# Kernel optimization log

Hardware: AMD Instinct MI355X
Metric: run time of the kernel (lower is better)

The kernel has to match this reference:

```python
import jax, jax.numpy as jnp
import numpy as np

B, L, NIN, NHID, NLAYERS = 16, 2048, 1024, 1024, 2


def _gru_step_zero_h(x, W_ih, b_ih, W_hh, b_hh):
    """torch GRU cell with h_prev = 0 (faithful to the module's bug where
    hidden is never updated and starts at zeros).
    r = sigmoid(W_ir x + b_ir + b_hr)
    z = sigmoid(W_iz x + b_iz + b_hz)
    n = tanh(W_in x + b_in + r * b_hn)   # W_hn @ 0 == 0
    h = (1 - z) * n                       # + z * 0
    W_hh is unused because h_prev == 0 (kept as an arg for parity).
    """
    del W_hh
    g = jnp.einsum('blf,hf->blh', x, W_ih) + b_ih  # (B, L, 3H)
    H = b_ih.shape[0] // 3
    gi_r, gi_z, gi_n = g[..., :H], g[..., H:2 * H], g[..., 2 * H:]
    bh_r, bh_z, bh_n = b_hh[:H], b_hh[H:2 * H], b_hh[2 * H:]
    r = jax.nn.sigmoid(gi_r + bh_r)
    z = jax.nn.sigmoid(gi_z + bh_z)
    n = jnp.tanh(gi_n + r * bh_n)
    return (1.0 - z) * n


def setup_inputs() -> dict:
    key = jax.random.key(0)
    ks = jax.random.split(key, 12)
    s_in = 1.0 / np.sqrt(NIN)
    s_h = 1.0 / np.sqrt(NHID)
    inp = {
        'inputs': jax.random.normal(ks[0], (B, L, NIN), dtype=jnp.float32),
        'inputs_mask': jax.random.randint(ks[1], (B, L), 0, 2, dtype=jnp.int32),
        # layer 0 (input size NIN)
        'W_ih0': jax.random.uniform(ks[2], (3 * NHID, NIN), jnp.float32, -s_in, s_in),
        'W_hh0': jax.random.uniform(ks[3], (3 * NHID, NHID), jnp.float32, -s_h, s_h),
        'b_ih0': jax.random.uniform(ks[4], (3 * NHID,), jnp.float32, -s_h, s_h),
        'b_hh0': jax.random.uniform(ks[5], (3 * NHID,), jnp.float32, -s_h, s_h),
        # layer 1 (input size NHID)
        'W_ih1': jax.random.uniform(ks[6], (3 * NHID, NHID), jnp.float32, -s_h, s_h),
        'W_hh1': jax.random.uniform(ks[7], (3 * NHID, NHID), jnp.float32, -s_h, s_h),
        'b_ih1': jax.random.uniform(ks[8], (3 * NHID,), jnp.float32, -s_h, s_h),
        'b_hh1': jax.random.uniform(ks[9], (3 * NHID,), jnp.float32, -s_h, s_h),
    }
    return inp


def reference(inputs, inputs_mask, W_ih0, W_hh0, b_ih0, b_hh0,
              W_ih1, W_hh1, b_ih1, b_hh1):
    # hidden is never updated in the original step(), so every timestep runs
    # the 2-layer GRU one step from zero hidden -> fully parallel over time.
    h1 = _gru_step_zero_h(inputs, W_ih0, b_ih0, W_hh0, b_hh0)   # (B, L, H)
    h2 = _gru_step_zero_h(h1, W_ih1, b_ih1, W_hh1, b_hh1)       # (B, L, H)
    mask = inputs_mask.astype(h2.dtype)[..., None]               # (B, L, 1)
    # output_p * mask + hidden[0] * (1 - mask), with hidden[0] == 0
    out = h2 * mask
    # original returns (steps, b_s, nhid)
    return jnp.transpose(out, (1, 0, 2))
```

## Files before the change

### kernel.cpp

```cpp
#include <hip/hip_runtime.h>
#include <hip/hip_bf16.h>
#include <cstdint>
#include <cstddef>

#define BB 16
#define LL 2048
#define MM (BB * LL)
#define KK 1024
#define HH 1024

typedef __attribute__((ext_vector_type(8))) short bf16x8;
typedef __attribute__((ext_vector_type(4))) float f32x4;

__device__ __forceinline__ unsigned short f2bf(float f) {
    unsigned u = __builtin_bit_cast(unsigned, f);
    u += 0x7fffu + ((u >> 16) & 1u);
    return (unsigned short)(u >> 16);
}

__global__ void cvt_f32_to_bf16(const float* __restrict__ in,
                                unsigned short* __restrict__ out, int n8) {
    int i = blockIdx.x * blockDim.x + threadIdx.x;
    if (i >= n8) return;
    const float4* p = reinterpret_cast<const float4*>(in) + (size_t)i * 2;
    float4 v0 = p[0];
    float4 v1 = p[1];
    union { unsigned short us[8]; uint4 v; } o;
    o.us[0] = f2bf(v0.x); o.us[1] = f2bf(v0.y);
    o.us[2] = f2bf(v0.z); o.us[3] = f2bf(v0.w);
    o.us[4] = f2bf(v1.x); o.us[5] = f2bf(v1.y);
    o.us[6] = f2bf(v1.z); o.us[7] = f2bf(v1.w);
    reinterpret_cast<uint4*>(out)[i] = o.v;
}

__global__ __launch_bounds__(1024) void scan_mask(const int* __restrict__ mask,
                                                  int* __restrict__ rows,
                                                  int* __restrict__ Na) {
    __shared__ int psum[1024];
    const int t = threadIdx.x;
    const int base = t * 32;
    int m[32];
    int cnt = 0;
#pragma unroll
    for (int i = 0; i < 32; ++i) { m[i] = mask[base + i]; cnt += (m[i] != 0); }
    psum[t] = cnt;
    __syncthreads();
    for (int off = 1; off < 1024; off <<= 1) {
        int v = (t >= off) ? psum[t - off] : 0;
        __syncthreads();
        psum[t] += v;
        __syncthreads();
    }
    int offset = psum[t] - cnt;
#pragma unroll
    for (int i = 0; i < 32; ++i) {
        if (m[i]) rows[offset++] = base + i;
    }
    if (t == 1023) *Na = psum[1023];
}

__global__ __launch_bounds__(256) void gather_cvt(const float* __restrict__ x,
                                                  const int* __restrict__ rows,
                                                  const int* __restrict__ Na,
                                                  unsigned short* __restrict__ xbf) {
    const int j = blockIdx.x;
    if (j >= *Na) return;
    const int r = rows[j];
    const float4 v = reinterpret_cast<const float4*>(x + (size_t)r * KK)[threadIdx.x];
    ushort4 o;
    o.x = f2bf(v.x); o.y = f2bf(v.y); o.z = f2bf(v.z); o.w = f2bf(v.w);
    reinterpret_cast<ushort4*>(xbf + (size_t)j * KK)[threadIdx.x] = o;
}

__global__ __launch_bounds__(256) void zero_masked(const int* __restrict__ mask,
                                                   float* __restrict__ out) {
    const int m = blockIdx.x;
    if (mask[m] != 0) return;
    const int bb = m >> 11;
    const int ll = m & 2047;
    float4 z = {0.f, 0.f, 0.f, 0.f};
    reinterpret_cast<float4*>(out + ((size_t)ll * BB + bb) * HH)[threadIdx.x] = z;
}

__device__ __forceinline__ void gload16(const unsigned short* g, unsigned short* l) {
    __builtin_amdgcn_global_load_lds(
        (const __attribute__((address_space(1))) unsigned int*)g,
        (__attribute__((address_space(3))) unsigned int*)l,
        16, 0, 0);
}

#define WAITVM0  asm volatile("s_waitcnt vmcnt(0)" ::: "memory")
#define SB       __builtin_amdgcn_sched_barrier(0)
#define BAR      __builtin_amdgcn_s_barrier()

template <int MODE>
__global__ __launch_bounds__(256, 3) void gru_layer(
    const unsigned short* __restrict__ A,
    const unsigned short* __restrict__ W,
    const float* __restrict__ b_ih,
    const float* __restrict__ b_hh,
    const int* __restrict__ rows,
    const int* __restrict__ Na_p,
    unsigned short* __restrict__ out_bf,
    float* __restrict__ out_f) {
    __shared__ unsigned short lds[2][10240];

    const int Na = *Na_p;
    const int m0 = blockIdx.x * 128;
    if (m0 >= Na) return;
    const int n0 = blockIdx.y * 64;

    const int tid  = threadIdx.x;
    const int lane = tid & 63;
    const int wid  = tid >> 6;
    const int wr   = wid >> 1;
    const int wc   = wid & 1;

    const int trow = tid >> 2;
    const int tcol = ((tid & 3) ^ ((trow >> 1) & 3)) * 8;
    int r0 = m0 + trow;        if (r0 >= Na) r0 = Na - 1;
    int r1 = m0 + 64 + trow;   if (r1 >= Na) r1 = Na - 1;
    const unsigned short* a0 = A + (size_t)r0 * KK + tcol;
    const unsigned short* a1 = A + (size_t)r1 * KK + tcol;
    const unsigned short* b0 = W + (size_t)(0 * HH + n0 + trow) * KK + tcol;
    const unsigned short* b1 = W + (size_t)(1 * HH + n0 + trow) * KK + tcol;
    const unsigned short* b2 = W + (size_t)(2 * HH + n0 + trow) * KK + tcol;

#define STAGE(kt, c) do {                                        \
        const int _o = (kt) * 32;                                \
        unsigned short* _L = &lds[(c)][wid * 512];               \
        gload16(a0 + _o, _L + 0 * 2048);                         \
        gload16(a1 + _o, _L + 1 * 2048);                         \
        gload16(b0 + _o, _L + 2 * 2048);                         \
        gload16(b1 + _o, _L + 3 * 2048);                         \
        gload16(b2 + _o, _L + 4 * 2048);                         \
    } while (0)

    const int l15 = lane & 15;
    const int akp = (((lane >> 4) ^ (lane >> 1)) & 3) << 3;
    int aoff[4], boff[2];
#pragma unroll
    for (int mf = 0; mf < 4; ++mf)
        aoff[mf] = (wr * 64 + mf * 16 + l15) * 32 + akp;
#pragma unroll
    for (int nf = 0; nf < 2; ++nf)
        boff[nf] = 4096 + (wc * 32 + nf * 16 + l15) * 32 + akp;

    f32x4 accr[4][2] = {};
    f32x4 accz[4][2] = {};
    f32x4 accn[4][2] = {};

#define COMPUTE(Lp) do {                                                          \
        bf16x8 af[4];                                                             \
        _Pragma("unroll") for (int mf = 0; mf < 4; ++mf)                          \
            af[mf] = *reinterpret_cast<const bf16x8*>(&(Lp)[aoff[mf]]);           \
        _Pragma("unroll") for (int nf = 0; nf < 2; ++nf) {                        \
            bf16x8 br  = *reinterpret_cast<const bf16x8*>(&(Lp)[boff[nf]]);       \
            bf16x8 bz  = *reinterpret_cast<const bf16x8*>(&(Lp)[boff[nf] + 2048]);\
            bf16x8 bnn = *reinterpret_cast<const bf16x8*>(&(Lp)[boff[nf] + 4096]);\
            __builtin_amdgcn_s_setprio(1);                                        \
            _Pragma("unroll") for (int mf = 0; mf < 4; ++mf) {                    \
                accr[mf][nf] = __builtin_amdgcn_mfma_f32_16x16x32_bf16(           \
                    af[mf], br,  accr[mf][nf], 0, 0, 0);                          \
                accz[mf][nf] = __builtin_amdgcn_mfma_f32_16x16x32_bf16(           \
                    af[mf], bz,  accz[mf][nf], 0, 0, 0);                          \
                accn[mf][nf] = __builtin_amdgcn_mfma_f32_16x16x32_bf16(           \
                    af[mf], bnn, accn[mf][nf], 0, 0, 0);                          \
            }                                                                     \
            __builtin_amdgcn_s_setprio(0);                                        \
        }                                                                         \
    } while (0)

    STAGE(0, 0);
    WAITVM0; BAR; SB;

    int cur = 0;
#pragma unroll 1
    for (int kt = 0; kt < 31; ++kt) {
        STAGE(kt + 1, cur ^ 1);
        const unsigned short* L = &lds[cur][0];
        COMPUTE(L);
        WAITVM0; BAR; SB;
        cur ^= 1;
    }
    {
        const unsigned short* L = &lds[cur][0];
        COMPUTE(L);
    }

#pragma unroll
    for (int nf = 0; nf < 2; ++nf) {
        const int col = n0 + wc * 32 + nf * 16 + l15;
        const float br_b = b_ih[col] + b_hh[col];
        const float bz_b = b_ih[HH + col] + b_hh[HH + col];
        const float bn_i = b_ih[2 * HH + col];
        const float bn_h = b_hh[2 * HH + col];
#pragma unroll
        for (int mf = 0; mf < 4; ++mf) {
#pragma unroll
            for (int j = 0; j < 4; ++j) {
                const int row = m0 + wr * 64 + mf * 16 + (lane >> 4) * 4 + j;
                if (row >= Na) continue;
                const float r = 1.f / (1.f + __expf(-(accr[mf][nf][j] + br_b)));
                const float z = 1.f / (1.f + __expf(-(accz[mf][nf][j] + bz_b)));
                const float n = tanhf(accn[mf][nf][j] + bn_i + r * bn_h);
                const float h = (1.f - z) * n;
                if (MODE == 0) {
                    out_bf[(size_t)row * HH + col] = f2bf(h);
                } else {
                    const int orig = rows[row];
                    const int bb = orig >> 11;
                    const int ll = orig & 2047;
                    out_f[((size_t)ll * BB + bb) * HH + col] = h;
                }
            }
        }
    }
#undef STAGE
#undef COMPUTE
}

extern "C" void kernel_launch(void* const* d_in, const int* in_sizes, int n_in,
                              void* d_out, int out_size, void* d_ws, size_t ws_size,
                              hipStream_t stream) {
    const float* x   = (const float*)d_in[0];
    const int*   msk = (const int*)d_in[1];
    const float* W0  = (const float*)d_in[2];
    const float* bi0 = (const float*)d_in[4];
    const float* bh0 = (const float*)d_in[5];
    const float* W1  = (const float*)d_in[6];
    const float* bi1 = (const float*)d_in[8];
    const float* bh1 = (const float*)d_in[9];
    float* out = (float*)d_out;

    char* ws = (char*)d_ws;
    unsigned short* xbf  = (unsigned short*)ws;
    unsigned short* h1bf = (unsigned short*)(ws + 67108864);
    unsigned short* w0bf = (unsigned short*)(ws + 134217728);
    unsigned short* w1bf = (unsigned short*)(ws + 140509184);
    int* rows = (int*)(ws + 146800640);
    int* Na   = (int*)(ws + 146931712);

    scan_mask<<<1, 1024, 0, stream>>>(msk, rows, Na);

    cvt_f32_to_bf16<<<1536, 256, 0, stream>>>(W0, w0bf, 3 * HH * KK / 8);
    cvt_f32_to_bf16<<<1536, 256, 0, stream>>>(W1, w1bf, 3 * HH * KK / 8);

    zero_masked<<<MM, 256, 0, stream>>>(msk, out);
    gather_cvt<<<MM, 256, 0, stream>>>(x, rows, Na, xbf);

    dim3 grid(MM / 128, HH / 64);
    gru_layer<0><<<grid, 256, 0, stream>>>(xbf, w0bf, bi0, bh0, rows, Na, h1bf, nullptr);
    gru_layer<1><<<grid, 256, 0, stream>>>(h1bf, w1bf, bi1, bh1, rows, Na, nullptr, out);
}
```

Measured before the change: 348.6 us.

## Double K-tile depth to 64 per stage with reworked LDS swizzle

Widens each pipeline stage from a K-slice of 32 to 64, doubling LDS buffers and halving the number of main-loop iterations and barriers. The LDS layout and XOR swizzle are redesigned for 64-element rows, and all fragments are loaded up front before issuing two MFMA passes. Fewer sync points and longer MFMA runs per stage are the goal, but LDS per block doubles and launch bounds drop occupancy from 3 to 2 blocks per CU, which reduces latency hiding.

```diff
diff --git a/kernel.cpp b/kernel.cpp
--- a/kernel.cpp
+++ b/kernel.cpp
@@ -94,7 +94,7 @@
 #define BAR      __builtin_amdgcn_s_barrier()
 
 template <int MODE>
-__global__ __launch_bounds__(256, 3) void gru_layer(
+__global__ __launch_bounds__(256, 2) void gru_layer(
     const unsigned short* __restrict__ A,
     const unsigned short* __restrict__ W,
     const float* __restrict__ b_ih,
@@ -103,7 +103,7 @@
     const int* __restrict__ Na_p,
     unsigned short* __restrict__ out_bf,
     float* __restrict__ out_f) {
-    __shared__ unsigned short lds[2][10240];
+    __shared__ unsigned short lds[2][20480];
 
     const int Na = *Na_p;
     const int m0 = blockIdx.x * 128;
@@ -116,59 +116,86 @@
     const int wr   = wid >> 1;
     const int wc   = wid & 1;
 
-    const int trow = tid >> 2;
-    const int tcol = ((tid & 3) ^ ((trow >> 1) & 3)) * 8;
-    int r0 = m0 + trow;        if (r0 >= Na) r0 = Na - 1;
-    int r1 = m0 + 64 + trow;   if (r1 >= Na) r1 = Na - 1;
-    const unsigned short* a0 = A + (size_t)r0 * KK + tcol;
-    const unsigned short* a1 = A + (size_t)r1 * KK + tcol;
-    const unsigned short* b0 = W + (size_t)(0 * HH + n0 + trow) * KK + tcol;
-    const unsigned short* b1 = W + (size_t)(1 * HH + n0 + trow) * KK + tcol;
-    const unsigned short* b2 = W + (size_t)(2 * HH + n0 + trow) * KK + tcol;
-
-#define STAGE(kt, c) do {                                        \
-        const int _o = (kt) * 32;                                \
-        unsigned short* _L = &lds[(c)][wid * 512];               \
-        gload16(a0 + _o, _L + 0 * 2048);                         \
-        gload16(a1 + _o, _L + 1 * 2048);                         \
-        gload16(b0 + _o, _L + 2 * 2048);                         \
-        gload16(b1 + _o, _L + 3 * 2048);                         \
-        gload16(b2 + _o, _L + 4 * 2048);                         \
+    const int trow = tid >> 3;
+    const int tcol = ((tid & 7) ^ (trow & 7)) * 8;
+    const unsigned short* ap[2][2];
+#pragma unroll
+    for (int u = 0; u < 2; ++u)
+#pragma unroll
+        for (int c = 0; c < 2; ++c) {
+            int r = m0 + u * 64 + c * 32 + trow;
+            if (r >= Na) r = Na - 1;
+            ap[u][c] = A + (size_t)r * KK + tcol;
+        }
+    const unsigned short* bp[3];
+#pragma unroll
+    for (int g = 0; g < 3; ++g)
+        bp[g] = W + (size_t)(g * HH + n0 + trow) * KK + tcol;
+
+#define STAGE(kt, buf) do {                                                   \
+        const int _o = (kt) * 64;                                             \
+        unsigned short* D = &lds[(buf)][wid * 512];                           \
+        gload16(ap[0][0] + _o, D + 0 * 4096 + 0 * 2048);                      \
+        gload16(ap[0][1] + _o, D + 0 * 4096 + 1 * 2048);                      \
+        gload16(ap[1][0] + _o, D + 1 * 4096 + 0 * 2048);                      \
+        gload16(ap[1][1] + _o, D + 1 * 4096 + 1 * 2048);                      \
+        gload16(bp[0] + _o, D + 2 * 4096 + 0 * 2048);                         \
+        gload16(bp[0] + 32 * KK + _o, D + 2 * 4096 + 1 * 2048);               \
+        gload16(bp[1] + _o, D + 3 * 4096 + 0 * 2048);                         \
+        gload16(bp[1] + 32 * KK + _o, D + 3 * 4096 + 1 * 2048);               \
+        gload16(bp[2] + _o, D + 4 * 4096 + 0 * 2048);                         \
+        gload16(bp[2] + 32 * KK + _o, D + 4 * 4096 + 1 * 2048);               \
     } while (0)
 
     const int l15 = lane & 15;
-    const int akp = (((lane >> 4) ^ (lane >> 1)) & 3) << 3;
-    int aoff[4], boff[2];
+    const int r7  = l15 & 7;
+    const int akp0 = (((0 * 4 + (lane >> 4)) ^ r7) << 3);
+    const int akp1 = (((1 * 4 + (lane >> 4)) ^ r7) << 3);
+    int aoff[4], boff[3];
 #pragma unroll
     for (int mf = 0; mf < 4; ++mf)
-        aoff[mf] = (wr * 64 + mf * 16 + l15) * 32 + akp;
-#pragma unroll
-    for (int nf = 0; nf < 2; ++nf)
-        boff[nf] = 4096 + (wc * 32 + nf * 16 + l15) * 32 + akp;
+        aoff[mf] = wr * 4096 + (mf * 16 + l15) * 64;
+#pragma unroll
+    for (int g = 0; g < 3; ++g)
+        boff[g] = (2 + g) * 4096 + (wc * 32 + l15) * 64;
 
     f32x4 accr[4][2] = {};
     f32x4 accz[4][2] = {};
     f32x4 accn[4][2] = {};
 
-#define COMPUTE(Lp) do {                                                          \
-        bf16x8 af[4];                                                             \
-        _Pragma("unroll") for (int mf = 0; mf < 4; ++mf)                          \
-            af[mf] = *reinterpret_cast<const bf16x8*>(&(Lp)[aoff[mf]]);           \
-        _Pragma("unroll") for (int nf = 0; nf < 2; ++nf) {                        \
-            bf16x8 br  = *reinterpret_cast<const bf16x8*>(&(Lp)[boff[nf]]);       \
-            bf16x8 bz  = *reinterpret_cast<const bf16x8*>(&(Lp)[boff[nf] + 2048]);\
-            bf16x8 bnn = *reinterpret_cast<const bf16x8*>(&(Lp)[boff[nf] + 4096]);\
-            __builtin_amdgcn_s_setprio(1);                                        \
-            _Pragma("unroll") for (int mf = 0; mf < 4; ++mf) {                    \
-                accr[mf][nf] = __builtin_amdgcn_mfma_f32_16x16x32_bf16(           \
-                    af[mf], br,  accr[mf][nf], 0, 0, 0);                          \
-                accz[mf][nf] = __builtin_amdgcn_mfma_f32_16x16x32_bf16(           \
-                    af[mf], bz,  accz[mf][nf], 0, 0, 0);                          \
-                accn[mf][nf] = __builtin_amdgcn_mfma_f32_16x16x32_bf16(           \
-                    af[mf], bnn, accn[mf][nf], 0, 0, 0);                          \
-            }                                                                     \
-            __builtin_amdgcn_s_setprio(0);                                        \
-        }                                                                         \
+#define COMPUTE(Lp) do {                                                           \
+        bf16x8 af0[4], af1[4], bfr0[2][3], bfr1[2][3];                             \
+        _Pragma("unroll") for (int mf = 0; mf < 4; ++mf) {                         \
+            af0[mf] = *reinterpret_cast<const bf16x8*>(&(Lp)[aoff[mf] + akp0]);    \
+            af1[mf] = *reinterpret_cast<const bf16x8*>(&(Lp)[aoff[mf] + akp1]);    \
+        }                                                                          \
+        _Pragma("unroll") for (int nf = 0; nf < 2; ++nf)                           \
+            _Pragma("unroll") for (int g = 0; g < 3; ++g) {                        \
+                bfr0[nf][g] = *reinterpret_cast<const bf16x8*>(                    \
+                    &(Lp)[boff[g] + nf * 1024 + akp0]);                            \
+                bfr1[nf][g] = *reinterpret_cast<const bf16x8*>(                    \
+                    &(Lp)[boff[g] + nf * 1024 + akp1]);                            \
+            }                                                                      \
+        __builtin_amdgcn_s_setprio(1);                                             \
+        _Pragma("unroll") for (int nf = 0; nf < 2; ++nf)                           \
+            _Pragma("unroll") for (int mf = 0; mf < 4; ++mf) {                     \
+                accr[mf][nf] = __builtin_amdgcn_mfma_f32_16x16x32_bf16(            \
+                    af0[mf], bfr0[nf][0], accr[mf][nf], 0, 0, 0);                  \
+                accz[mf][nf] = __builtin_amdgcn_mfma_f32_16x16x32_bf16(            \
+                    af0[mf], bfr0[nf][1], accz[mf][nf], 0, 0, 0);                  \
+                accn[mf][nf] = __builtin_amdgcn_mfma_f32_16x16x32_bf16(            \
+                    af0[mf], bfr0[nf][2], accn[mf][nf], 0, 0, 0);                  \
+            }                                                                      \
+        _Pragma("unroll") for (int nf = 0; nf < 2; ++nf)                           \
+            _Pragma("unroll") for (int mf = 0; mf < 4; ++mf) {                     \
+                accr[mf][nf] = __builtin_amdgcn_mfma_f32_16x16x32_bf16(            \
+                    af1[mf], bfr1[nf][0], accr[mf][nf], 0, 0, 0);                  \
+                accz[mf][nf] = __builtin_amdgcn_mfma_f32_16x16x32_bf16(            \
+                    af1[mf], bfr1[nf][1], accz[mf][nf], 0, 0, 0);                  \
+                accn[mf][nf] = __builtin_amdgcn_mfma_f32_16x16x32_bf16(            \
+                    af1[mf], bfr1[nf][2], accn[mf][nf], 0, 0, 0);                  \
+            }                                                                      \
+        __builtin_amdgcn_s_setprio(0);                                             \
     } while (0)
 
     STAGE(0, 0);
@@ -176,7 +203,7 @@
 
     int cur = 0;
 #pragma unroll 1
-    for (int kt = 0; kt < 31; ++kt) {
+    for (int kt = 0; kt < 15; ++kt) {
         STAGE(kt + 1, cur ^ 1);
         const unsigned short* L = &lds[cur][0];
         COMPUTE(L);
```

Result: slower. 366.8 us (+5.2%).

## Shrink GRU GEMM tile to 32 hidden columns and raise occupancy to 4 waves

Applied to the files above, without the earlier changes.

Halves the per-block hidden-column tile from 64 to 32, so each block stages 128 rows of A and 96 rows of W (three gates) per k-step, which cuts LDS to 32 KB and accumulators to 12 per thread. The launch bound is raised to 4 blocks per SM and the grid doubles along the hidden dimension. The aim is more occupancy and latency hiding, at the cost of lower arithmetic intensity: the A tile is reloaded twice as often.

```diff
diff --git a/kernel.cpp b/kernel.cpp
--- a/kernel.cpp
+++ b/kernel.cpp
@@ -94,7 +94,7 @@
 #define BAR      __builtin_amdgcn_s_barrier()
 
 template <int MODE>
-__global__ __launch_bounds__(256, 3) void gru_layer(
+__global__ __launch_bounds__(256, 4) void gru_layer(
     const unsigned short* __restrict__ A,
     const unsigned short* __restrict__ W,
     const float* __restrict__ b_ih,
@@ -103,12 +103,12 @@
     const int* __restrict__ Na_p,
     unsigned short* __restrict__ out_bf,
     float* __restrict__ out_f) {
-    __shared__ unsigned short lds[2][10240];
+    __shared__ unsigned short lds[2][8192];
 
     const int Na = *Na_p;
     const int m0 = blockIdx.x * 128;
     if (m0 >= Na) return;
-    const int n0 = blockIdx.y * 64;
+    const int n0 = blockIdx.y * 32;
 
     const int tid  = threadIdx.x;
     const int lane = tid & 63;
@@ -120,55 +120,45 @@
     const int tcol = ((tid & 3) ^ ((trow >> 1) & 3)) * 8;
     int r0 = m0 + trow;        if (r0 >= Na) r0 = Na - 1;
     int r1 = m0 + 64 + trow;   if (r1 >= Na) r1 = Na - 1;
-    const unsigned short* a0 = A + (size_t)r0 * KK + tcol;
-    const unsigned short* a1 = A + (size_t)r1 * KK + tcol;
-    const unsigned short* b0 = W + (size_t)(0 * HH + n0 + trow) * KK + tcol;
-    const unsigned short* b1 = W + (size_t)(1 * HH + n0 + trow) * KK + tcol;
-    const unsigned short* b2 = W + (size_t)(2 * HH + n0 + trow) * KK + tcol;
-
-#define STAGE(kt, c) do {                                        \
-        const int _o = (kt) * 32;                                \
-        unsigned short* _L = &lds[(c)][wid * 512];               \
-        gload16(a0 + _o, _L + 0 * 2048);                         \
-        gload16(a1 + _o, _L + 1 * 2048);                         \
-        gload16(b0 + _o, _L + 2 * 2048);                         \
-        gload16(b1 + _o, _L + 3 * 2048);                         \
-        gload16(b2 + _o, _L + 4 * 2048);                         \
+    const unsigned short* aA = A + (size_t)r0 * KK + tcol;
+    const unsigned short* aB = A + (size_t)r1 * KK + tcol;
+    const int b01row = (trow < 32) ? (0 * HH + n0 + trow) : (1 * HH + n0 + trow - 32);
+    const unsigned short* b01 = W + (size_t)b01row * KK + tcol;
+    const unsigned short* b2d = W + (size_t)(2 * HH + n0 + (trow & 31)) * KK + tcol;
+
+#define STAGE(kt, buf) do {                                   \
+        const int _o = (kt) * 32;                             \
+        unsigned short* D = &lds[(buf)][wid * 512];           \
+        gload16(aA  + _o, D + 0);                             \
+        gload16(aB  + _o, D + 2048);                          \
+        gload16(b01 + _o, D + 4096);                          \
+        gload16(b2d + _o, D + 6144);                          \
     } while (0)
 
     const int l15 = lane & 15;
     const int akp = (((lane >> 4) ^ (lane >> 1)) & 3) << 3;
-    int aoff[4], boff[2];
+    int aoff[4], boff[3];
 #pragma unroll
     for (int mf = 0; mf < 4; ++mf)
         aoff[mf] = (wr * 64 + mf * 16 + l15) * 32 + akp;
 #pragma unroll
-    for (int nf = 0; nf < 2; ++nf)
-        boff[nf] = 4096 + (wc * 32 + nf * 16 + l15) * 32 + akp;
-
-    f32x4 accr[4][2] = {};
-    f32x4 accz[4][2] = {};
-    f32x4 accn[4][2] = {};
+    for (int g = 0; g < 3; ++g)
+        boff[g] = 4096 + (g * 32 + wc * 16 + l15) * 32 + akp;
+
+    f32x4 acc[4][3] = {};
 
 #define COMPUTE(Lp) do {                                                          \
-        bf16x8 af[4];                                                             \
+        bf16x8 af[4], bf[3];                                                      \
         _Pragma("unroll") for (int mf = 0; mf < 4; ++mf)                          \
             af[mf] = *reinterpret_cast<const bf16x8*>(&(Lp)[aoff[mf]]);           \
-        _Pragma("unroll") for (int nf = 0; nf < 2; ++nf) {                        \
-            bf16x8 br  = *reinterpret_cast<const bf16x8*>(&(Lp)[boff[nf]]);       \
-            bf16x8 bz  = *reinterpret_cast<const bf16x8*>(&(Lp)[boff[nf] + 2048]);\
-            bf16x8 bnn = *reinterpret_cast<const bf16x8*>(&(Lp)[boff[nf] + 4096]);\
-            __builtin_amdgcn_s_setprio(1);                                        \
-            _Pragma("unroll") for (int mf = 0; mf < 4; ++mf) {                    \
-                accr[mf][nf] = __builtin_amdgcn_mfma_f32_16x16x32_bf16(           \
-                    af[mf], br,  accr[mf][nf], 0, 0, 0);                          \
-                accz[mf][nf] = __builtin_amdgcn_mfma_f32_16x16x32_bf16(           \
-                    af[mf], bz,  accz[mf][nf], 0, 0, 0);                          \
-                accn[mf][nf] = __builtin_amdgcn_mfma_f32_16x16x32_bf16(           \
-                    af[mf], bnn, accn[mf][nf], 0, 0, 0);                          \
-            }                                                                     \
-            __builtin_amdgcn_s_setprio(0);                                        \
-        }                                                                         \
+        _Pragma("unroll") for (int g = 0; g < 3; ++g)                             \
+            bf[g] = *reinterpret_cast<const bf16x8*>(&(Lp)[boff[g]]);             \
+        __builtin_amdgcn_s_setprio(1);                                            \
+        _Pragma("unroll") for (int g = 0; g < 3; ++g)                             \
+            _Pragma("unroll") for (int mf = 0; mf < 4; ++mf)                      \
+                acc[mf][g] = __builtin_amdgcn_mfma_f32_16x16x32_bf16(             \
+                    af[mf], bf[g], acc[mf][g], 0, 0, 0);                          \
+        __builtin_amdgcn_s_setprio(0);                                            \
     } while (0)
 
     STAGE(0, 0);
@@ -188,31 +178,28 @@
         COMPUTE(L);
     }
 
-#pragma unroll
-    for (int nf = 0; nf < 2; ++nf) {
-        const int col = n0 + wc * 32 + nf * 16 + l15;
-        const float br_b = b_ih[col] + b_hh[col];
-        const float bz_b = b_ih[HH + col] + b_hh[HH + col];
-        const float bn_i = b_ih[2 * HH + col];
-        const float bn_h = b_hh[2 * HH + col];
-#pragma unroll
-        for (int mf = 0; mf < 4; ++mf) {
-#pragma unroll
-            for (int j = 0; j < 4; ++j) {
-                const int row = m0 + wr * 64 + mf * 16 + (lane >> 4) * 4 + j;
-                if (row >= Na) continue;
-                const float r = 1.f / (1.f + __expf(-(accr[mf][nf][j] + br_b)));
-                const float z = 1.f / (1.f + __expf(-(accz[mf][nf][j] + bz_b)));
-                const float n = tanhf(accn[mf][nf][j] + bn_i + r * bn_h);
-                const float h = (1.f - z) * n;
-                if (MODE == 0) {
-                    out_bf[(size_t)row * HH + col] = f2bf(h);
-                } else {
-                    const int orig = rows[row];
-                    const int bb = orig >> 11;
-                    const int ll = orig & 2047;
-                    out_f[((size_t)ll * BB + bb) * HH + col] = h;
-                }
+    const int col = n0 + wc * 16 + l15;
+    const float br_b = b_ih[col] + b_hh[col];
+    const float bz_b = b_ih[HH + col] + b_hh[HH + col];
+    const float bn_i = b_ih[2 * HH + col];
+    const float bn_h = b_hh[2 * HH + col];
+#pragma unroll
+    for (int mf = 0; mf < 4; ++mf) {
+#pragma unroll
+        for (int j = 0; j < 4; ++j) {
+            const int row = m0 + wr * 64 + mf * 16 + (lane >> 4) * 4 + j;
+            if (row >= Na) continue;
+            const float r = 1.f / (1.f + __expf(-(acc[mf][0][j] + br_b)));
+            const float z = 1.f / (1.f + __expf(-(acc[mf][1][j] + bz_b)));
+            const float n = tanhf(acc[mf][2][j] + bn_i + r * bn_h);
+            const float h = (1.f - z) * n;
+            if (MODE == 0) {
+                out_bf[(size_t)row * HH + col] = f2bf(h);
+            } else {
+                const int orig = rows[row];
+                const int bb = orig >> 11;
+                const int ll = orig & 2047;
+                out_f[((size_t)ll * BB + bb) * HH + col] = h;
             }
         }
     }
@@ -249,7 +236,7 @@
     zero_masked<<<MM, 256, 0, stream>>>(msk, out);
     gather_cvt<<<MM, 256, 0, stream>>>(x, rows, Na, xbf);
 
-    dim3 grid(MM / 128, HH / 64);
+    dim3 grid(MM / 128, HH / 32);
     gru_layer<0><<<grid, 256, 0, stream>>>(xbf, w0bf, bi0, bh0, rows, Na, h1bf, nullptr);
     gru_layer<1><<<grid, 256, 0, stream>>>(h1bf, w1bf, bi1, bh1, rows, Na, nullptr, out);
 }
```

Measured after the change: 385.9 us. 10.7% more time.

## Triple-buffer LDS K-tiles with partial vmcnt waits in GRU GEMM

Applied to the files above, without the earlier changes.

Replaces the double-buffered LDS pipeline with a three-stage ring. Each step waits only for the older tile (vmcnt(5)) and prefetches two tiles ahead, so global loads overlap more of the MFMA compute. The K loop is unrolled by three with fixed buffer indices, and launch bounds drop from three to two blocks per CU to fit the extra LDS. The trade is lower occupancy in return for deeper prefetch.

```diff
diff --git a/kernel.cpp b/kernel.cpp
--- a/kernel.cpp
+++ b/kernel.cpp
@@ -89,12 +89,13 @@
         16, 0, 0);
 }
 
+#define WAITVM5  asm volatile("s_waitcnt vmcnt(5)" ::: "memory")
 #define WAITVM0  asm volatile("s_waitcnt vmcnt(0)" ::: "memory")
 #define SB       __builtin_amdgcn_sched_barrier(0)
 #define BAR      __builtin_amdgcn_s_barrier()
 
 template <int MODE>
-__global__ __launch_bounds__(256, 3) void gru_layer(
+__global__ __launch_bounds__(256, 2) void gru_layer(
     const unsigned short* __restrict__ A,
     const unsigned short* __restrict__ W,
     const float* __restrict__ b_ih,
@@ -103,7 +104,7 @@
     const int* __restrict__ Na_p,
     unsigned short* __restrict__ out_bf,
     float* __restrict__ out_f) {
-    __shared__ unsigned short lds[2][10240];
+    __shared__ unsigned short lds[3][10240];
 
     const int Na = *Na_p;
     const int m0 = blockIdx.x * 128;
@@ -126,9 +127,9 @@
     const unsigned short* b1 = W + (size_t)(1 * HH + n0 + trow) * KK + tcol;
     const unsigned short* b2 = W + (size_t)(2 * HH + n0 + trow) * KK + tcol;
 
-#define STAGE(kt, c) do {                                        \
+#define STAGE(kt, Lb) do {                                       \
         const int _o = (kt) * 32;                                \
-        unsigned short* _L = &lds[(c)][wid * 512];               \
+        unsigned short* _L = (Lb) + wid * 512;                   \
         gload16(a0 + _o, _L + 0 * 2048);                         \
         gload16(a1 + _o, _L + 1 * 2048);                         \
         gload16(b0 + _o, _L + 2 * 2048);                         \
@@ -171,22 +172,25 @@
         }                                                                         \
     } while (0)
 
-    STAGE(0, 0);
+#define TILE(kt, cb, sb) do {                                  \
+        WAITVM5; BAR; SB;                                      \
+        STAGE((kt) + 2, &lds[(sb)][0]);                        \
+        COMPUTE((&lds[(cb)][0]));                              \
+    } while (0)
+
+    STAGE(0, &lds[0][0]);
+    STAGE(1, &lds[1][0]);
+
+#pragma unroll 1
+    for (int kt3 = 0; kt3 < 30; kt3 += 3) {
+        TILE(kt3 + 0, 0, 2);
+        TILE(kt3 + 1, 1, 0);
+        TILE(kt3 + 2, 2, 1);
+    }
+    WAITVM5; BAR; SB;
+    COMPUTE((&lds[0][0]));
     WAITVM0; BAR; SB;
-
-    int cur = 0;
-#pragma unroll 1
-    for (int kt = 0; kt < 31; ++kt) {
-        STAGE(kt + 1, cur ^ 1);
-        const unsigned short* L = &lds[cur][0];
-        COMPUTE(L);
-        WAITVM0; BAR; SB;
-        cur ^= 1;
-    }
-    {
-        const unsigned short* L = &lds[cur][0];
-        COMPUTE(L);
-    }
+    COMPUTE((&lds[1][0]));
 
 #pragma unroll
     for (int nf = 0; nf < 2; ++nf) {
@@ -218,6 +222,7 @@
     }
 #undef STAGE
 #undef COMPUTE
+#undef TILE
 }
 
 extern "C" void kernel_launch(void* const* d_in, const int* in_sizes, int n_in,
```

Result: slower. 370.2 us (+6.2%).
